# Kernel tuning notes

Measured on AMD Instinct MI355X. Metric: run time of the kernel, lower is better.

## Reference

```python
import jax, jax.numpy as jnp
import numpy as np

IMAGE_SIZE = 256  # init kwarg image_size
BS, NCAM, N = 2, 3, 128


def _normalise_scale_factor(v):
    v = v / v.mean()
    sf = 0.2 / jnp.abs(v - 1.0).max()
    return jnp.where(sf < 1.0, (v - 1.0) * sf + 1.0, v)


def setup_inputs() -> dict:
    key = jax.random.key(0)
    ks = jax.random.split(key, 7)
    S = IMAGE_SIZE
    # 2D projected points in pixel coords [0, S)
    points = jax.random.uniform(ks[0], (BS, NCAM, N, 2), dtype=jnp.float32) * S
    # per-point render params in the model's clamp ranges
    sigmas = jax.random.uniform(ks[1], (BS, N), dtype=jnp.float32) * 0.06 + 0.041
    exponents = jax.random.uniform(ks[2], (BS, N), dtype=jnp.float32) * 1.5 + 0.5
    intensities = jax.random.uniform(ks[3], (BS, N), dtype=jnp.float32) * 0.6 + 0.41
    # per-camera scale factors near 1
    camera_sigmas = jax.random.uniform(ks[4], (BS, NCAM), dtype=jnp.float32) * 0.2 + 0.9
    camera_exponents = jax.random.uniform(ks[5], (BS, NCAM), dtype=jnp.float32) * 0.2 + 0.9
    camera_intensities = jax.random.uniform(ks[6], (BS, NCAM), dtype=jnp.float32) * 0.2 + 0.9
    return {
        'points': points, 'sigmas': sigmas, 'exponents': exponents,
        'intensities': intensities, 'camera_sigmas': camera_sigmas,
        'camera_exponents': camera_exponents, 'camera_intensities': camera_intensities,
    }


def reference(points, sigmas, exponents, intensities,
              camera_sigmas, camera_exponents, camera_intensities):
    S = IMAGE_SIZE
    bs, N = points.shape[0], points.shape[2]
    s2 = S // 2
    # normalise pixel coords to [-1, 1], flatten cameras into batch
    p = jnp.clip((points - s2) / s2, -1.0, 1.0).reshape(bs * 3, N, 2)
    # camera scale factors (normalised as in forward())
    cs = _normalise_scale_factor(camera_sigmas).reshape(bs * 3)
    ce = _normalise_scale_factor(camera_exponents).reshape(bs * 3)
    ci = _normalise_scale_factor(camera_intensities).reshape(bs * 3)
    # repeat_interleave(3, 0) over batch -> (bs*3, N, 1, 1)
    sig = (jnp.repeat(sigmas, 3, axis=0) * cs[:, None])[:, :, None, None]
    expn = (jnp.repeat(exponents, 3, axis=0) * ce[:, None])[:, :, None, None]
    inten = (jnp.repeat(intensities, 3, axis=0) * ci[:, None])[:, :, None, None]
    grid = jnp.linspace(-1.0, 1.0, S, dtype=jnp.float32)
    px = p[:, :, 0][:, :, None, None]  # (bs3, N, 1, 1)
    py = p[:, :, 1][:, :, None, None]
    # squared distance of every point to every pixel: (bs3, N, S, S)
    # y varies over axis -2 (rows), x over axis -1 (cols), matching meshgrid(ij)
    dst = (grid[None, None, None, :] - px) ** 2 + (grid[None, None, :, None] - py) ** 2
    blobs = jnp.exp(-(dst / (2.0 * sig ** 2)) ** expn)
    masks = jnp.minimum((blobs * inten).max(axis=1), 1.0)  # amax over N points
    masks = masks.reshape(bs, 3, S, S)
    blobs = blobs.reshape(bs, 3, N, S, S)
    return masks, blobs
```

## Files before the change

### kernel.cpp

```cpp
#include <hip/hip_runtime.h>

#define SZ   256
#define NPTS 128
#define NB3  6

#define EXP2F(x) __builtin_amdgcn_exp2f(x)
#define LOG2F(x) __builtin_amdgcn_logf(x)

__device__ __forceinline__ float norm6(const float* __restrict__ v, int idx) {
    float a0 = v[0], a1 = v[1], a2 = v[2], a3 = v[3], a4 = v[4], a5 = v[5];
    float mean = (a0 + a1 + a2 + a3 + a4 + a5) * (1.0f / 6.0f);
    float inv = 1.0f / mean;
    float b0 = a0 * inv, b1 = a1 * inv, b2 = a2 * inv;
    float b3 = a3 * inv, b4 = a4 * inv, b5 = a5 * inv;
    float d = fmaxf(fmaxf(fmaxf(fabsf(b0 - 1.f), fabsf(b1 - 1.f)),
                          fmaxf(fabsf(b2 - 1.f), fabsf(b3 - 1.f))),
                    fmaxf(fabsf(b4 - 1.f), fabsf(b5 - 1.f)));
    float sf = 0.2f / d;
    float vi = v[idx] * inv;
    return (sf < 1.0f) ? (vi - 1.0f) * sf + 1.0f : vi;
}

__global__ __launch_bounds__(256) void render_kernel(
    const float* __restrict__ points,
    const float* __restrict__ sigmas,
    const float* __restrict__ exponents,
    const float* __restrict__ intensities,
    const float* __restrict__ cam_s,
    const float* __restrict__ cam_e,
    const float* __restrict__ cam_i,
    float* __restrict__ masks,
    float* __restrict__ blobs)
{
    __shared__ float4 s_p[NPTS];
    __shared__ float  s_i[NPTS];

    const int b3  = blockIdx.x >> 8;
    const int y   = blockIdx.x & 255;
    const int tid = threadIdx.x;

    if (tid < NPTS) {
        const int b = b3 / 3;
        const float cs = norm6(cam_s, b3);
        const float ce = norm6(cam_e, b3);
        const float ci = norm6(cam_i, b3);
        float px = points[(b3 * NPTS + tid) * 2 + 0];
        float py = points[(b3 * NPTS + tid) * 2 + 1];
        px = fminf(fmaxf((px - 128.0f) * (1.0f / 128.0f), -1.0f), 1.0f);
        py = fminf(fmaxf((py - 128.0f) * (1.0f / 128.0f), -1.0f), 1.0f);
        const float sg = sigmas[b * NPTS + tid] * cs;
        const float e  = exponents[b * NPTS + tid] * ce;
        const float q  = 1.0f / (2.0f * sg * sg);
        const float C  = 0.5287663729448977f;
        const float c2 = fmaf(e, LOG2F(q), C);
        s_p[tid] = make_float4(px, py, e, c2);
        s_i[tid] = intensities[b * NPTS + tid] * ci;
    }
    __syncthreads();

    const float gy = -1.0f + (float)y   * (2.0f / 255.0f);
    const float gx = -1.0f + (float)tid * (2.0f / 255.0f);

    float m = 0.0f;
    float* bptr = blobs + (size_t)b3 * NPTS * SZ * SZ + (size_t)y * SZ + tid;

    #pragma unroll 4
    for (int n = 0; n < NPTS; ++n) {
        const float4 p = s_p[n];
        const float dx = gx - p.x;
        const float dy = gy - p.y;
        const float u  = fmaf(dx, dx, dy * dy);
        const float l  = fmaf(p.z, LOG2F(u), p.w);
        const float t  = EXP2F(l);
        const float bl = EXP2F(-t);
        bptr[(size_t)n * (SZ * SZ)] = bl;
        m = fmaxf(m, bl * s_i[n]);
    }

    masks[(size_t)b3 * SZ * SZ + (size_t)y * SZ + tid] = fminf(m, 1.0f);
}

extern "C" void kernel_launch(void* const* d_in, const int* in_sizes, int n_in,
                              void* d_out, int out_size, void* d_ws, size_t ws_size,
                              hipStream_t stream) {
    const float* points      = (const float*)d_in[0];
    const float* sigmas      = (const float*)d_in[1];
    const float* exponents   = (const float*)d_in[2];
    const float* intensities = (const float*)d_in[3];
    const float* cam_s       = (const float*)d_in[4];
    const float* cam_e       = (const float*)d_in[5];
    const float* cam_i       = (const float*)d_in[6];

    float* out   = (float*)d_out;
    float* masks = out;
    float* blobs = out + NB3 * SZ * SZ;

    hipLaunchKernelGGL(render_kernel, dim3(NB3 * SZ), dim3(256), 0, stream,
                       points, sigmas, exponents, intensities,
                       cam_s, cam_e, cam_i, masks, blobs);
}
```

Baseline: 208.3 us.

## Split blob writing into a per-point kernel with contiguous vector nontemporal stores

Blob writing moves into its own kernel with one block per (camera-batch, point) pair. Each thread computes four adjacent pixels and writes 64 rows with 16-byte nontemporal stores, so each point's image plane is written contiguously. The old per-row kernel wrote scattered 1 KB rows across 128 planes. A separate masks kernel now recomputes every blob value without storing it. This doubles the transcendental work and adds a second launch in exchange for a better write pattern on the roughly 200 MB output.

```diff
diff --git a/kernel.cpp b/kernel.cpp
--- a/kernel.cpp
+++ b/kernel.cpp
@@ -6,6 +6,8 @@
 
 #define EXP2F(x) __builtin_amdgcn_exp2f(x)
 #define LOG2F(x) __builtin_amdgcn_logf(x)
+
+typedef float v4f __attribute__((ext_vector_type(4)));
 
 __device__ __forceinline__ float norm6(const float* __restrict__ v, int idx) {
     float a0 = v[0], a1 = v[1], a2 = v[2], a3 = v[3], a4 = v[4], a5 = v[5];
@@ -21,7 +23,65 @@
     return (sf < 1.0f) ? (vi - 1.0f) * sf + 1.0f : vi;
 }
 
-__global__ __launch_bounds__(256) void render_kernel(
+
+__global__ __launch_bounds__(256) void blobs_kernel(
+    const float* __restrict__ points,
+    const float* __restrict__ sigmas,
+    const float* __restrict__ exponents,
+    const float* __restrict__ cam_s,
+    const float* __restrict__ cam_e,
+    float* __restrict__ blobs)
+{
+    const int n   = blockIdx.x & 127;
+    const int b3  = blockIdx.x >> 7;
+    const int b   = b3 / 3;
+    const int tid = threadIdx.x;
+    const int w   = tid >> 6;
+    const int ln  = tid & 63;
+
+    const float cs = norm6(cam_s, b3);
+    const float ce = norm6(cam_e, b3);
+    float px = points[(b3 * NPTS + n) * 2 + 0];
+    float py = points[(b3 * NPTS + n) * 2 + 1];
+    px = fminf(fmaxf((px - 128.0f) * (1.0f / 128.0f), -1.0f), 1.0f);
+    py = fminf(fmaxf((py - 128.0f) * (1.0f / 128.0f), -1.0f), 1.0f);
+    const float sg = sigmas[b * NPTS + n] * cs;
+    const float e  = exponents[b * NPTS + n] * ce;
+    const float q  = 1.0f / (2.0f * sg * sg);
+    const float C  = 0.5287663729448977f;
+    const float c2 = fmaf(e, LOG2F(q), C);
+
+    const int x = ln << 2;
+    const float dx0 = (-1.0f + (float)(x + 0) * (2.0f / 255.0f)) - px;
+    const float dx1 = (-1.0f + (float)(x + 1) * (2.0f / 255.0f)) - px;
+    const float dx2 = (-1.0f + (float)(x + 2) * (2.0f / 255.0f)) - px;
+    const float dx3 = (-1.0f + (float)(x + 3) * (2.0f / 255.0f)) - px;
+    const float q0 = dx0 * dx0, q1 = dx1 * dx1;
+    const float q2 = dx2 * dx2, q3 = dx3 * dx3;
+
+    const int y0 = w << 6;
+    v4f* bp = (v4f*)(blobs + (size_t)(b3 * NPTS + n) * (SZ * SZ)
+                           + (size_t)y0 * SZ + x);
+
+    #pragma unroll 4
+    for (int r = 0; r < 64; ++r) {
+        const float gy  = -1.0f + (float)(y0 + r) * (2.0f / 255.0f);
+        const float dy  = gy - py;
+        const float dy2 = dy * dy;
+        const float u0 = q0 + dy2, u1 = q1 + dy2;
+        const float u2 = q2 + dy2, u3 = q3 + dy2;
+        const float t0 = EXP2F(fmaf(e, LOG2F(u0), c2));
+        const float t1 = EXP2F(fmaf(e, LOG2F(u1), c2));
+        const float t2 = EXP2F(fmaf(e, LOG2F(u2), c2));
+        const float t3 = EXP2F(fmaf(e, LOG2F(u3), c2));
+        v4f out_v;
+        out_v.x = EXP2F(-t0); out_v.y = EXP2F(-t1);
+        out_v.z = EXP2F(-t2); out_v.w = EXP2F(-t3);
+        __builtin_nontemporal_store(out_v, bp + (size_t)r * (SZ / 4));
+    }
+}
+
+__global__ __launch_bounds__(256) void masks_kernel(
     const float* __restrict__ points,
     const float* __restrict__ sigmas,
     const float* __restrict__ exponents,
@@ -29,8 +89,7 @@
     const float* __restrict__ cam_s,
     const float* __restrict__ cam_e,
     const float* __restrict__ cam_i,
-    float* __restrict__ masks,
-    float* __restrict__ blobs)
+    float* __restrict__ masks)
 {
     __shared__ float4 s_p[NPTS];
     __shared__ float  s_i[NPTS];
@@ -62,8 +121,6 @@
     const float gx = -1.0f + (float)tid * (2.0f / 255.0f);
 
     float m = 0.0f;
-    float* bptr = blobs + (size_t)b3 * NPTS * SZ * SZ + (size_t)y * SZ + tid;
-
     #pragma unroll 4
     for (int n = 0; n < NPTS; ++n) {
         const float4 p = s_p[n];
@@ -73,10 +130,8 @@
         const float l  = fmaf(p.z, LOG2F(u), p.w);
         const float t  = EXP2F(l);
         const float bl = EXP2F(-t);
-        bptr[(size_t)n * (SZ * SZ)] = bl;
         m = fmaxf(m, bl * s_i[n]);
     }
-
     masks[(size_t)b3 * SZ * SZ + (size_t)y * SZ + tid] = fminf(m, 1.0f);
 }
 
@@ -95,7 +150,9 @@
     float* masks = out;
     float* blobs = out + NB3 * SZ * SZ;
 
-    hipLaunchKernelGGL(render_kernel, dim3(NB3 * SZ), dim3(256), 0, stream,
+    hipLaunchKernelGGL(blobs_kernel, dim3(NB3 * NPTS), dim3(256), 0, stream,
+                       points, sigmas, exponents, cam_s, cam_e, blobs);
+    hipLaunchKernelGGL(masks_kernel, dim3(NB3 * SZ), dim3(256), 0, stream,
                        points, sigmas, exponents, intensities,
-                       cam_s, cam_e, cam_i, masks, blobs);
+                       cam_s, cam_e, cam_i, masks);
 }
```

Measured after the change: 236.2 us. +13.4%, slower.
